# Optimization experiments

Measured on AMD Instinct MI355X. Metric: run time of the kernel, lower is better.

## Reference

```python
import jax, jax.numpy as jnp
import numpy as np

H = 8        # num_heads
D = 64       # qkv_dim
E = 512      # embed_dim = H*D
MS = 16      # ms_hidden_dim


def setup_inputs() -> dict:
    key = jax.random.key(0)
    ks = jax.random.split(key, 12)
    b, r, c = 4, 512, 512
    row_emb = jax.random.normal(ks[0], (b, r, E), dtype=jnp.float32)
    col_emb = jax.random.normal(ks[1], (b, c, E), dtype=jnp.float32)
    cost_mat = jax.random.uniform(ks[2], (b, r, c), dtype=jnp.float32)
    attn_mask = jax.random.randint(ks[3], (b, H, r, c), 0, 2) > 0
    s = 1.0 / np.sqrt(E)
    Wq = jax.random.uniform(ks[4], (H * D, E), minval=-s, maxval=s)
    Wk = jax.random.uniform(ks[5], (H * D, E), minval=-s, maxval=s)
    Wv = jax.random.uniform(ks[6], (H * D, E), minval=-s, maxval=s)
    Wout = jax.random.uniform(ks[7], (E, E), minval=-s, maxval=s)
    m1 = np.sqrt(0.5)
    m2 = np.sqrt(1.0 / MS)
    Wmix1 = jax.random.uniform(ks[8], (H * MS, 2 * H), minval=-m1, maxval=m1)
    Wmix2 = jax.random.uniform(ks[9], (H, H * MS), minval=-m2, maxval=m2)
    return {"row_emb": row_emb, "col_emb": col_emb, "cost_mat": cost_mat,
            "attn_mask": attn_mask, "Wq": Wq, "Wk": Wk, "Wv": Wv,
            "Wmix1": Wmix1, "Wmix2": Wmix2, "Wout": Wout}


def reference(row_emb, col_emb, cost_mat, attn_mask, Wq, Wk, Wv, Wmix1, Wmix2, Wout):
    b, r, _ = row_emb.shape
    c = col_emb.shape[1]
    norm = 1.0 / jnp.sqrt(jnp.asarray(D, row_emb.dtype))
    # projections -> [b, h, s, d]
    q = (row_emb @ Wq.T).reshape(b, r, H, D).transpose(0, 2, 1, 3)
    k = (col_emb @ Wk.T).reshape(b, c, H, D).transpose(0, 2, 1, 3)
    v = (col_emb @ Wv.T).reshape(b, c, H, D).transpose(0, 2, 1, 3)
    dot = norm * jnp.einsum('bhrd,bhcd->bhrc', q, k)            # [b,h,r,c]
    cost = jnp.broadcast_to(cost_mat[:, None, :, :], dot.shape)  # [b,h,r,c]
    # stack then rearrange 'b h r c s -> b r c (h s)' (h major, s minor)
    two = jnp.stack([dot, cost], axis=-1)                        # [b,h,r,c,2]
    two = two.transpose(0, 2, 3, 1, 4).reshape(b, r, c, 2 * H)
    hid = jax.nn.relu(two @ Wmix1.T)                             # [b,r,c,H*MS]
    ms = hid @ Wmix2.T                                           # [b,r,c,H]
    logits = ms.transpose(0, 3, 1, 2)                            # [b,h,r,c]
    # mask handling: rows that are fully masked become fully unmasked
    all_masked = jnp.all(attn_mask, axis=-1, keepdims=True)
    mask = jnp.where(all_masked, False, attn_mask)
    logits = jnp.where(mask, -jnp.inf, logits)
    weights = jax.nn.softmax(logits, axis=-1)
    out = jnp.einsum('bhrc,bhcd->bhrd', weights, v)              # [b,h,r,d]
    out = out.transpose(0, 2, 1, 3).reshape(b, r, H * D)         # b s (h d)
    return out @ Wout.T
```

## Files before the change

kernel.cpp:

```cpp
#include <hip/hip_runtime.h>
#include <math.h>

typedef __attribute__((ext_vector_type(8))) short bf16x8;
typedef __attribute__((ext_vector_type(4))) float f32x4;
typedef unsigned short ushort_t;

static __device__ inline unsigned short f2bf(float f) {
    union { float f; unsigned u; } v; v.f = f;
    unsigned r = v.u + 0x7fff + ((v.u >> 16) & 1);
    return (unsigned short)(r >> 16);
}

#if defined(__has_builtin)
#  if __has_builtin(__builtin_amdgcn_cvt_pk_bf16_f32)
#    define HAVE_PK_BF16 1
#  endif
#endif

static __device__ inline unsigned pk2bf(float a, float b) {
#ifdef HAVE_PK_BF16
    auto r = __builtin_amdgcn_cvt_pk_bf16_f32(a, b);
    unsigned u; __builtin_memcpy(&u, &r, 4);
    return u;
#else
    return (unsigned)f2bf(a) | ((unsigned)f2bf(b) << 16);
#endif
}

__global__ __launch_bounds__(256) void convert_allm(const float* __restrict__ a0,
                                                    const float* __restrict__ a1,
                                                    const float* __restrict__ a2,
                                                    const float* __restrict__ a3,
                                                    const float* __restrict__ a4,
                                                    const float* __restrict__ a5,
                                                    const int* __restrict__ mask,
                                                    ushort_t* __restrict__ dst,
                                                    int* __restrict__ allmOut) {
    if (blockIdx.x < 3072) {
        const size_t e = ((size_t)blockIdx.x * 256 + threadIdx.x) * 4;
        const float* src; size_t off;
        if      (e < 1048576) { src = a0; off = 0; }
        else if (e < 2097152) { src = a1; off = 1048576; }
        else if (e < 2359296) { src = a2; off = 2097152; }
        else if (e < 2621440) { src = a3; off = 2359296; }
        else if (e < 2883584) { src = a4; off = 2621440; }
        else                  { src = a5; off = 2883584; }
        const float4 v = *(const float4*)(src + (e - off));
        uint2 o; o.x = pk2bf(v.x, v.y); o.y = pk2bf(v.z, v.w);
        *(uint2*)(dst + e) = o;
    } else {
        const int bid  = blockIdx.x - 3072;
        const int w    = threadIdx.x >> 6;
        const int lane = threadIdx.x & 63;
        const int row  = bid * 4 + w;
        const int* mp = mask + (size_t)row * 512 + lane * 8;
        const int4 m0 = *(const int4*)mp;
        const int4 m1 = *(const int4*)(mp + 4);
        const int allv = (m0.x && m0.y && m0.z && m0.w &&
                          m1.x && m1.y && m1.z && m1.w);
        const int res = (__all(allv) != 0) ? 1 : 0;
        if (lane == 0) allmOut[row] = res;
    }
}

__global__ __launch_bounds__(256) void gemm_qkv(const ushort_t* __restrict__ rowb,
                                                const ushort_t* __restrict__ colb,
                                                const ushort_t* __restrict__ Wqb,
                                                const ushort_t* __restrict__ Wkb,
                                                const ushort_t* __restrict__ Wvb,
                                                ushort_t* __restrict__ Qb,
                                                ushort_t* __restrict__ Kb,
                                                ushort_t* __restrict__ Vt) {
    const int z = blockIdx.z;
    const ushort_t* A = (z == 0) ? rowb : colb;
    const ushort_t* B = (z == 0) ? Wqb : (z == 1) ? Wkb : Wvb;

    const int t    = threadIdx.x;
    const int w    = t >> 6;
    const int lane = t & 63;
    const int quad = lane >> 4;
    const int sl   = lane & 15;
    const int m0 = blockIdx.x * 64 + (w >> 1) * 32;
    const int n0 = blockIdx.y * 64 + (w & 1) * 32;

    const ushort_t* ap0 = A + (size_t)(m0 + sl) * 512 + quad * 8;
    const ushort_t* ap1 = A + (size_t)(m0 + 16 + sl) * 512 + quad * 8;
    const ushort_t* bp0 = B + (size_t)(n0 + sl) * 512 + quad * 8;
    const ushort_t* bp1 = B + (size_t)(n0 + 16 + sl) * 512 + quad * 8;

    f32x4 acc[2][2] = {};

    bf16x8 a0 = *(const bf16x8*)ap0;
    bf16x8 a1 = *(const bf16x8*)ap1;
    bf16x8 b0 = *(const bf16x8*)bp0;
    bf16x8 b1 = *(const bf16x8*)bp1;

    for (int ks = 0; ks < 16; ++ks) {
        bf16x8 na0, na1, nb0, nb1;
        if (ks < 15) {
            const int k0 = (ks + 1) * 32;
            na0 = *(const bf16x8*)(ap0 + k0);
            na1 = *(const bf16x8*)(ap1 + k0);
            nb0 = *(const bf16x8*)(bp0 + k0);
            nb1 = *(const bf16x8*)(bp1 + k0);
        }
        acc[0][0] = __builtin_amdgcn_mfma_f32_16x16x32_bf16(a0, b0, acc[0][0], 0, 0, 0);
        acc[0][1] = __builtin_amdgcn_mfma_f32_16x16x32_bf16(a0, b1, acc[0][1], 0, 0, 0);
        acc[1][0] = __builtin_amdgcn_mfma_f32_16x16x32_bf16(a1, b0, acc[1][0], 0, 0, 0);
        acc[1][1] = __builtin_amdgcn_mfma_f32_16x16x32_bf16(a1, b1, acc[1][1], 0, 0, 0);
        a0 = na0; a1 = na1; b0 = nb0; b1 = nb1;
    }

#pragma unroll
    for (int rs = 0; rs < 2; ++rs)
#pragma unroll
        for (int cs = 0; cs < 2; ++cs) {
            const int n = n0 + cs * 16 + sl;
            if (z == 2) {
                const int mb   = m0 + rs * 16 + quad * 4;
                const int bidx = mb >> 9, c = mb & 511;
                const int h = n >> 6, d = n & 63;
                ushort4 o;
                o.x = f2bf(acc[rs][cs][0]); o.y = f2bf(acc[rs][cs][1]);
                o.z = f2bf(acc[rs][cs][2]); o.w = f2bf(acc[rs][cs][3]);
                *(ushort4*)(Vt + (size_t)(((bidx * 8 + h) * 64 + d)) * 512 + c) = o;
            } else {
                ushort_t* C = (z == 0) ? Qb : Kb;
#pragma unroll
                for (int reg = 0; reg < 4; ++reg) {
                    const int m = m0 + rs * 16 + quad * 4 + reg;
                    C[(size_t)m * 512 + n] = f2bf(acc[rs][cs][reg]);
                }
            }
        }
}

__global__ __launch_bounds__(256) void gemm_out(const ushort_t* __restrict__ A,
                                                const ushort_t* __restrict__ B,
                                                float* __restrict__ C) {
    const int t    = threadIdx.x;
    const int w    = t >> 6;
    const int lane = t & 63;
    const int quad = lane >> 4;
    const int sl   = lane & 15;
    const int m0 = blockIdx.x * 64 + (w >> 1) * 32;
    const int n0 = blockIdx.y * 64 + (w & 1) * 32;

    const ushort_t* ap0 = A + (size_t)(m0 + sl) * 512 + quad * 8;
    const ushort_t* ap1 = A + (size_t)(m0 + 16 + sl) * 512 + quad * 8;
    const ushort_t* bp0 = B + (size_t)(n0 + sl) * 512 + quad * 8;
    const ushort_t* bp1 = B + (size_t)(n0 + 16 + sl) * 512 + quad * 8;

    f32x4 acc[2][2] = {};

    bf16x8 a0 = *(const bf16x8*)ap0;
    bf16x8 a1 = *(const bf16x8*)ap1;
    bf16x8 b0 = *(const bf16x8*)bp0;
    bf16x8 b1 = *(const bf16x8*)bp1;

    for (int ks = 0; ks < 16; ++ks) {
        bf16x8 na0, na1, nb0, nb1;
        if (ks < 15) {
            const int k0 = (ks + 1) * 32;
            na0 = *(const bf16x8*)(ap0 + k0);
            na1 = *(const bf16x8*)(ap1 + k0);
            nb0 = *(const bf16x8*)(bp0 + k0);
            nb1 = *(const bf16x8*)(bp1 + k0);
        }
        acc[0][0] = __builtin_amdgcn_mfma_f32_16x16x32_bf16(a0, b0, acc[0][0], 0, 0, 0);
        acc[0][1] = __builtin_amdgcn_mfma_f32_16x16x32_bf16(a0, b1, acc[0][1], 0, 0, 0);
        acc[1][0] = __builtin_amdgcn_mfma_f32_16x16x32_bf16(a1, b0, acc[1][0], 0, 0, 0);
        acc[1][1] = __builtin_amdgcn_mfma_f32_16x16x32_bf16(a1, b1, acc[1][1], 0, 0, 0);
        a0 = na0; a1 = na1; b0 = nb0; b1 = nb1;
    }

#pragma unroll
    for (int rs = 0; rs < 2; ++rs)
#pragma unroll
        for (int cs = 0; cs < 2; ++cs) {
            const int n = n0 + cs * 16 + sl;
#pragma unroll
            for (int reg = 0; reg < 4; ++reg) {
                const int m = m0 + rs * 16 + quad * 4 + reg;
                C[(size_t)m * 512 + n] = acc[rs][cs][reg];
            }
        }
}

__global__ __launch_bounds__(512) void dot_mlp_v7(const ushort_t* __restrict__ Qb,
                                                  const ushort_t* __restrict__ Kb,
                                                  const float* __restrict__ cost,
                                                  const float* __restrict__ W1,
                                                  const float* __restrict__ W2,
                                                  const int* __restrict__ mask,
                                                  const int* __restrict__ allm,
                                                  ushort_t* __restrict__ tbuf,
                                                  float* __restrict__ lpart) {
    __shared__ ushort_t Xs[1024 * 18];
    __shared__ ushort_t hidS[8 * 16 * 36];
    __shared__ ushort_t W1fs[128 * 16];
    __shared__ ushort_t W2ss[8 * 128];

    const int b  = blockIdx.z;
    const int r0 = blockIdx.y * 32;
    const int c0 = blockIdx.x * 32;
    const int t    = threadIdx.x;
    const int w    = t >> 6;
    const int lane = t & 63;
    const int quad = lane >> 4;
    const int sl   = lane & 15;

    const bf16x8 zf = {0, 0, 0, 0, 0, 0, 0, 0};

    if (t < 128) {
        float s = 0.f;
#pragma unroll
        for (int h = 0; h < 8; ++h) {
            W1fs[t * 16 + h] = f2bf(W1[t * 16 + 2 * h]);
            s += W1[t * 16 + 2 * h + 1];
        }
        W1fs[t * 16 + 8] = f2bf(s);
#pragma unroll
        for (int k = 9; k < 16; ++k) W1fs[t * 16 + k] = 0;
    }
#pragma unroll
    for (int i = 0; i < 2; ++i) W2ss[t + i * 512] = f2bf(W2[t + i * 512]);

#pragma unroll
    for (int i = 0; i < 2; ++i) {
        const int cell = t + i * 512;
        const int rl = cell >> 5, cl = cell & 31;
        unsigned* base = (unsigned*)(Xs + cell * 18 + 8);
        base[0] = (unsigned)f2bf(cost[((size_t)b * 512 + r0 + rl) * 512 + c0 + cl]);
        base[1] = 0; base[2] = 0; base[3] = 0; base[4] = 0;
    }

    {
        const int hp = w & 3;
        const int h0 = hp * 2;
        const int rs = w >> 2;
        bf16x8 af[2][2], bfr[2][2][2];
#pragma unroll
        for (int hh = 0; hh < 2; ++hh)
#pragma unroll
            for (int ks = 0; ks < 2; ++ks) {
                af[hh][ks] = *(const bf16x8*)(Qb +
                    ((size_t)(b * 512 + r0 + rs * 16 + sl) * 512 + (h0 + hh) * 64 + ks * 32 + quad * 8));
#pragma unroll
                for (int cs = 0; cs < 2; ++cs)
                    bfr[hh][cs][ks] = *(const bf16x8*)(Kb +
                        ((size_t)(b * 512 + c0 + cs * 16 + sl) * 512 + (h0 + hh) * 64 + ks * 32 + quad * 8));
            }
        f32x4 dacc[2][2];
#pragma unroll
        for (int hh = 0; hh < 2; ++hh)
#pragma unroll
            for (int cs = 0; cs < 2; ++cs) {
                f32x4 acc = {0.f, 0.f, 0.f, 0.f};
                acc = __builtin_amdgcn_mfma_f32_16x16x32_bf16(af[hh][0], bfr[hh][cs][0], acc, 0, 0, 0);
                acc = __builtin_amdgcn_mfma_f32_16x16x32_bf16(af[hh][1], bfr[hh][cs][1], acc, 0, 0, 0);
                dacc[hh][cs] = acc;
            }
#pragma unroll
        for (int cs = 0; cs < 2; ++cs)
#pragma unroll
            for (int reg = 0; reg < 4; ++reg) {
                const int cell = (rs * 16 + quad * 4 + reg) * 32 + cs * 16 + sl;
                ((unsigned*)Xs)[cell * 9 + hp] =
                    pk2bf(dacc[0][cs][reg] * 0.125f, dacc[1][cs][reg] * 0.125f);
            }
    }

    __syncthreads();

    bf16x8 bw1[8];
#pragma unroll
    for (int nt = 0; nt < 8; ++nt)
        bw1[nt] = (quad < 2) ? *(const bf16x8*)&W1fs[(nt * 16 + sl) * 16 + quad * 8] : zf;
    bf16x8 bw2[4];
#pragma unroll
    for (int ks = 0; ks < 4; ++ks) {
        union { ushort_t s[8]; bf16x8 v; } tu;
#pragma unroll
        for (int i = 0; i < 8; ++i) {
            const int p  = quad * 8 + i;
            const int jc = (p >> 1) | ((p & 1) << 4);
            tu.s[i] = (sl < 8) ? W2ss[sl * 128 + ks * 32 + jc] : (ushort_t)0;
        }
        bw2[ks] = tu.v;
    }

    ushort_t* hidW = hidS + w * (16 * 36);

    float rsum[4] = {0.f, 0.f, 0.f, 0.f};

#pragma unroll
    for (int mt = 0; mt < 8; ++mt) {
        const int gmt = w * 8 + mt;
        const int cb  = gmt * 16;

        bf16x8 a1 = zf;
        if (quad < 2) {
            const unsigned* xr = (const unsigned*)Xs + (size_t)(cb + sl) * 9 + quad * 4;
            union { unsigned u[4]; bf16x8 v; } tmp;
            tmp.u[0] = xr[0]; tmp.u[1] = xr[1]; tmp.u[2] = xr[2]; tmp.u[3] = xr[3];
            a1 = tmp.v;
        }

        f32x4 acc2 = {0.f, 0.f, 0.f, 0.f};
#pragma unroll
        for (int ks = 0; ks < 4; ++ks) {
            f32x4 z = {0.f, 0.f, 0.f, 0.f};
            const f32x4 h0 = __builtin_amdgcn_mfma_f32_16x16x32_bf16(a1, bw1[2 * ks],     z, 0, 0, 0);
            const f32x4 h1 = __builtin_amdgcn_mfma_f32_16x16x32_bf16(a1, bw1[2 * ks + 1], z, 0, 0, 0);
#pragma unroll
            for (int rp = 0; rp < 4; ++rp)
                ((unsigned*)hidW)[(quad * 4 + rp) * 18 + sl] =
                    pk2bf(fmaxf(h0[rp], 0.f), fmaxf(h1[rp], 0.f));
            union { uint2 u2[2]; bf16x8 v; } tu;
            const ushort_t* hp2 = hidW + sl * 36 + quad * 8;
            tu.u2[0] = *(const uint2*)hp2;
            tu.u2[1] = *(const uint2*)(hp2 + 4);
            acc2 = __builtin_amdgcn_mfma_f32_16x16x32_bf16(tu.v, bw2[ks], acc2, 0, 0, 0);
        }

        float psum = 0.f;
        if (sl < 8) {
            const int r = r0 + (gmt >> 1);
            const int cbase = c0 + (gmt & 1) * 16 + quad * 4;
            const size_t rowoff = (size_t)(b * 8 + sl) * 512 + r;
            const int4 m4 = *(const int4*)(mask + rowoff * 512 + cbase);
            const int av = allm[rowoff];
            float tv0 = (av || !m4.x) ? __expf(acc2[0]) : 0.f;
            float tv1 = (av || !m4.y) ? __expf(acc2[1]) : 0.f;
            float tv2 = (av || !m4.z) ? __expf(acc2[2]) : 0.f;
            float tv3 = (av || !m4.w) ? __expf(acc2[3]) : 0.f;
            ushort4 o;
            o.x = f2bf(tv0); o.y = f2bf(tv1); o.z = f2bf(tv2); o.w = f2bf(tv3);
            *(ushort4*)&tbuf[rowoff * 512 + cbase] = o;
            psum = tv0 + tv1 + tv2 + tv3;
        }
        psum += __shfl_xor(psum, 16, 64);
        psum += __shfl_xor(psum, 32, 64);
        rsum[mt >> 1] += psum;
    }

    if (quad == 0 && sl < 8) {
#pragma unroll
        for (int i = 0; i < 4; ++i) {
            const size_t rowoff = (size_t)(b * 8 + sl) * 512 + (r0 + w * 4 + i);
            lpart[rowoff * 16 + blockIdx.x] = rsum[i];
        }
    }
}

__global__ __launch_bounds__(256) void pv_norm(const ushort_t* __restrict__ tbuf,
                                               const float* __restrict__ lpart,
                                               const ushort_t* __restrict__ Vt,
                                               ushort_t* __restrict__ Aout) {
    __shared__ float lsum[16];

    const int t    = threadIdx.x;
    const int w    = t >> 6;
    const int lane = t & 63;
    const int quad = lane >> 4;
    const int sl   = lane & 15;
    const int rt = blockIdx.x;
    const int bh = blockIdx.y;
    const int r0 = rt * 16;

    if (t < 16) {
        const float* lp = lpart + ((size_t)bh * 512 + r0 + t) * 16;
        const float4 s0 = *(const float4*)lp;
        const float4 s1 = *(const float4*)(lp + 4);
        const float4 s2 = *(const float4*)(lp + 8);
        const float4 s3 = *(const float4*)(lp + 12);
        lsum[t] = (s0.x + s0.y + s0.z + s0.w) + (s1.x + s1.y + s1.z + s1.w) +
                  (s2.x + s2.y + s2.z + s2.w) + (s3.x + s3.y + s3.z + s3.w);
    }
    __syncthreads();

    const ushort_t* tb = tbuf + (size_t)bh * 512 * 512;
    const ushort_t* vb = Vt + (size_t)bh * 64 * 512;
    const int n0w = w * 16;

    f32x4 acc = {0.f, 0.f, 0.f, 0.f};
    for (int ks = 0; ks < 16; ++ks) {
        const bf16x8 ta = *(const bf16x8*)(tb + (size_t)(r0 + sl) * 512 + ks * 32 + quad * 8);
        const bf16x8 bv = *(const bf16x8*)(vb + (size_t)(n0w + sl) * 512 + ks * 32 + quad * 8);
        acc = __builtin_amdgcn_mfma_f32_16x16x32_bf16(ta, bv, acc, 0, 0, 0);
    }

    const int bidx = bh >> 3, h = bh & 7;
    ushort_t* Cb = Aout + (size_t)bidx * 512 * 512 + h * 64;
    const int n = n0w + sl;
#pragma unroll
    for (int reg = 0; reg < 4; ++reg) {
        const int m = r0 + quad * 4 + reg;
        const float inv = 1.f / lsum[quad * 4 + reg];
        Cb[(size_t)m * 512 + n] = f2bf(acc[reg] * inv);
    }
}

extern "C" void kernel_launch(void* const* d_in, const int* in_sizes, int n_in,
                              void* d_out, int out_size, void* d_ws, size_t ws_size,
                              hipStream_t stream) {
    const float* row_emb = (const float*)d_in[0];
    const float* col_emb = (const float*)d_in[1];
    const float* cost    = (const float*)d_in[2];
    const int*   mask    = (const int*)d_in[3];
    const float* Wq      = (const float*)d_in[4];
    const float* Wk      = (const float*)d_in[5];
    const float* Wv      = (const float*)d_in[6];
    const float* Wmix1   = (const float*)d_in[7];
    const float* Wmix2   = (const float*)d_in[8];
    const float* Wout    = (const float*)d_in[9];
    float* out = (float*)d_out;

    char* ws = (char*)d_ws;
    const size_t MB = (size_t)1 << 20;
    ushort_t* convDst = (ushort_t*)ws;
    ushort_t* rowb  = (ushort_t*)(ws);
    ushort_t* colb  = (ushort_t*)(ws + 2 * MB);
    ushort_t* Wqb   = (ushort_t*)(ws + 4 * MB);
    ushort_t* Wkb   = (ushort_t*)(ws + 4 * MB + 512 * 1024);
    ushort_t* Wvb   = (ushort_t*)(ws + 5 * MB);
    ushort_t* Woutb = (ushort_t*)(ws + 5 * MB + 512 * 1024);
    ushort_t* Qb    = (ushort_t*)(ws + 6 * MB);
    ushort_t* Kb    = (ushort_t*)(ws + 8 * MB);
    ushort_t* Vt    = (ushort_t*)(ws + 10 * MB);
    ushort_t* Aoutb = (ushort_t*)(ws + 12 * MB);
    ushort_t* tbuf  = (ushort_t*)(ws + 16 * MB);
    float* lpart    = (float*)(ws + 34 * MB);
    int* allmBuf    = (int*)(ws + 35 * MB);

    convert_allm<<<7168, 256, 0, stream>>>(row_emb, col_emb, Wq, Wk, Wv, Wout,
                                           mask, convDst, allmBuf);

    gemm_qkv<<<dim3(32, 8, 3), 256, 0, stream>>>(rowb, colb, Wqb, Wkb, Wvb, Qb, Kb, Vt);

    dot_mlp_v7<<<dim3(16, 16, 4), 512, 0, stream>>>(Qb, Kb, cost, Wmix1, Wmix2,
                                                    mask, allmBuf, tbuf, lpart);

    pv_norm<<<dim3(32, 32), 256, 0, stream>>>(tbuf, lpart, Vt, Aoutb);

    gemm_out<<<dim3(32, 8), 256, 0, stream>>>(Aoutb, Woutb, out);
}
```

Baseline: 193.2 us.

## Pack attention mask into bitmask, split-K accumulators in GEMMs, smaller gemm_out tiles

The mask pre-pass now packs each row's int32 mask into a bitmask with the fully-masked-row rule folded in, so the MLP/softmax kernel reads one 32-bit word instead of an int4 plus a separate flag. That cuts mask traffic in the hot kernel roughly 32-fold. Both GEMMs split K into two independent accumulator chains to expose more MFMA parallelism and in-flight loads. gemm_out also drops to 32x32 tiles, launching four times as many blocks for better occupancy, at the cost of less operand reuse.

```diff
diff --git a/kernel.cpp b/kernel.cpp
--- a/kernel.cpp
+++ b/kernel.cpp
@@ -35,7 +35,7 @@
                                                     const float* __restrict__ a5,
                                                     const int* __restrict__ mask,
                                                     ushort_t* __restrict__ dst,
-                                                    int* __restrict__ allmOut) {
+                                                    unsigned char* __restrict__ bmask) {
     if (blockIdx.x < 3072) {
         const size_t e = ((size_t)blockIdx.x * 256 + threadIdx.x) * 4;
         const float* src; size_t off;
@@ -56,10 +56,17 @@
         const int* mp = mask + (size_t)row * 512 + lane * 8;
         const int4 m0 = *(const int4*)mp;
         const int4 m1 = *(const int4*)(mp + 4);
-        const int allv = (m0.x && m0.y && m0.z && m0.w &&
-                          m1.x && m1.y && m1.z && m1.w);
-        const int res = (__all(allv) != 0) ? 1 : 0;
-        if (lane == 0) allmOut[row] = res;
+        unsigned bits = 0;
+        bits |= (m0.x != 0) ? 1u   : 0u;
+        bits |= (m0.y != 0) ? 2u   : 0u;
+        bits |= (m0.z != 0) ? 4u   : 0u;
+        bits |= (m0.w != 0) ? 8u   : 0u;
+        bits |= (m1.x != 0) ? 16u  : 0u;
+        bits |= (m1.y != 0) ? 32u  : 0u;
+        bits |= (m1.z != 0) ? 64u  : 0u;
+        bits |= (m1.w != 0) ? 128u : 0u;
+        const bool all_masked = (__all(bits == 255u) != 0);
+        bmask[(size_t)row * 64 + lane] = all_masked ? 0 : (unsigned char)bits;
     }
 }
 
@@ -88,48 +95,54 @@
     const ushort_t* bp0 = B + (size_t)(n0 + sl) * 512 + quad * 8;
     const ushort_t* bp1 = B + (size_t)(n0 + 16 + sl) * 512 + quad * 8;
 
-    f32x4 acc[2][2] = {};
-
-    bf16x8 a0 = *(const bf16x8*)ap0;
-    bf16x8 a1 = *(const bf16x8*)ap1;
-    bf16x8 b0 = *(const bf16x8*)bp0;
-    bf16x8 b1 = *(const bf16x8*)bp1;
-
-    for (int ks = 0; ks < 16; ++ks) {
-        bf16x8 na0, na1, nb0, nb1;
-        if (ks < 15) {
-            const int k0 = (ks + 1) * 32;
-            na0 = *(const bf16x8*)(ap0 + k0);
-            na1 = *(const bf16x8*)(ap1 + k0);
-            nb0 = *(const bf16x8*)(bp0 + k0);
-            nb1 = *(const bf16x8*)(bp1 + k0);
-        }
-        acc[0][0] = __builtin_amdgcn_mfma_f32_16x16x32_bf16(a0, b0, acc[0][0], 0, 0, 0);
-        acc[0][1] = __builtin_amdgcn_mfma_f32_16x16x32_bf16(a0, b1, acc[0][1], 0, 0, 0);
-        acc[1][0] = __builtin_amdgcn_mfma_f32_16x16x32_bf16(a1, b0, acc[1][0], 0, 0, 0);
-        acc[1][1] = __builtin_amdgcn_mfma_f32_16x16x32_bf16(a1, b1, acc[1][1], 0, 0, 0);
-        a0 = na0; a1 = na1; b0 = nb0; b1 = nb1;
+    f32x4 accA[2][2] = {}, accB[2][2] = {};
+
+    bf16x8 a0A = *(const bf16x8*)ap0,         a1A = *(const bf16x8*)ap1;
+    bf16x8 b0A = *(const bf16x8*)bp0,         b1A = *(const bf16x8*)bp1;
+    bf16x8 a0B = *(const bf16x8*)(ap0 + 256), a1B = *(const bf16x8*)(ap1 + 256);
+    bf16x8 b0B = *(const bf16x8*)(bp0 + 256), b1B = *(const bf16x8*)(bp1 + 256);
+
+    for (int ks = 0; ks < 8; ++ks) {
+        bf16x8 na0A, na1A, nb0A, nb1A, na0B, na1B, nb0B, nb1B;
+        if (ks < 7) {
+            const int o = (ks + 1) * 32;
+            na0A = *(const bf16x8*)(ap0 + o);       na1A = *(const bf16x8*)(ap1 + o);
+            nb0A = *(const bf16x8*)(bp0 + o);       nb1A = *(const bf16x8*)(bp1 + o);
+            na0B = *(const bf16x8*)(ap0 + 256 + o); na1B = *(const bf16x8*)(ap1 + 256 + o);
+            nb0B = *(const bf16x8*)(bp0 + 256 + o); nb1B = *(const bf16x8*)(bp1 + 256 + o);
+        }
+        accA[0][0] = __builtin_amdgcn_mfma_f32_16x16x32_bf16(a0A, b0A, accA[0][0], 0, 0, 0);
+        accA[0][1] = __builtin_amdgcn_mfma_f32_16x16x32_bf16(a0A, b1A, accA[0][1], 0, 0, 0);
+        accA[1][0] = __builtin_amdgcn_mfma_f32_16x16x32_bf16(a1A, b0A, accA[1][0], 0, 0, 0);
+        accA[1][1] = __builtin_amdgcn_mfma_f32_16x16x32_bf16(a1A, b1A, accA[1][1], 0, 0, 0);
+        accB[0][0] = __builtin_amdgcn_mfma_f32_16x16x32_bf16(a0B, b0B, accB[0][0], 0, 0, 0);
+        accB[0][1] = __builtin_amdgcn_mfma_f32_16x16x32_bf16(a0B, b1B, accB[0][1], 0, 0, 0);
+        accB[1][0] = __builtin_amdgcn_mfma_f32_16x16x32_bf16(a1B, b0B, accB[1][0], 0, 0, 0);
+        accB[1][1] = __builtin_amdgcn_mfma_f32_16x16x32_bf16(a1B, b1B, accB[1][1], 0, 0, 0);
+        a0A = na0A; a1A = na1A; b0A = nb0A; b1A = nb1A;
+        a0B = na0B; a1B = na1B; b0B = nb0B; b1B = nb1B;
     }
 
 #pragma unroll
     for (int rs = 0; rs < 2; ++rs)
 #pragma unroll
         for (int cs = 0; cs < 2; ++cs) {
+            const f32x4 acc = accA[rs][cs] + accB[rs][cs];
             const int n = n0 + cs * 16 + sl;
             if (z == 2) {
                 const int mb   = m0 + rs * 16 + quad * 4;
                 const int bidx = mb >> 9, c = mb & 511;
                 const int h = n >> 6, d = n & 63;
                 ushort4 o;
-                o.x = f2bf(acc[rs][cs][0]); o.y = f2bf(acc[rs][cs][1]);
-                o.z = f2bf(acc[rs][cs][2]); o.w = f2bf(acc[rs][cs][3]);
+                o.x = f2bf(acc[0]); o.y = f2bf(acc[1]);
+                o.z = f2bf(acc[2]); o.w = f2bf(acc[3]);
                 *(ushort4*)(Vt + (size_t)(((bidx * 8 + h) * 64 + d)) * 512 + c) = o;
             } else {
                 ushort_t* C = (z == 0) ? Qb : Kb;
 #pragma unroll
                 for (int reg = 0; reg < 4; ++reg) {
                     const int m = m0 + rs * 16 + quad * 4 + reg;
-                    C[(size_t)m * 512 + n] = f2bf(acc[rs][cs][reg]);
+                    C[(size_t)m * 512 + n] = f2bf(acc[reg]);
                 }
             }
         }
@@ -143,57 +156,44 @@
     const int lane = t & 63;
     const int quad = lane >> 4;
     const int sl   = lane & 15;
-    const int m0 = blockIdx.x * 64 + (w >> 1) * 32;
-    const int n0 = blockIdx.y * 64 + (w & 1) * 32;
-
-    const ushort_t* ap0 = A + (size_t)(m0 + sl) * 512 + quad * 8;
-    const ushort_t* ap1 = A + (size_t)(m0 + 16 + sl) * 512 + quad * 8;
-    const ushort_t* bp0 = B + (size_t)(n0 + sl) * 512 + quad * 8;
-    const ushort_t* bp1 = B + (size_t)(n0 + 16 + sl) * 512 + quad * 8;
-
-    f32x4 acc[2][2] = {};
-
-    bf16x8 a0 = *(const bf16x8*)ap0;
-    bf16x8 a1 = *(const bf16x8*)ap1;
-    bf16x8 b0 = *(const bf16x8*)bp0;
-    bf16x8 b1 = *(const bf16x8*)bp1;
-
-    for (int ks = 0; ks < 16; ++ks) {
-        bf16x8 na0, na1, nb0, nb1;
-        if (ks < 15) {
-            const int k0 = (ks + 1) * 32;
-            na0 = *(const bf16x8*)(ap0 + k0);
-            na1 = *(const bf16x8*)(ap1 + k0);
-            nb0 = *(const bf16x8*)(bp0 + k0);
-            nb1 = *(const bf16x8*)(bp1 + k0);
-        }
-        acc[0][0] = __builtin_amdgcn_mfma_f32_16x16x32_bf16(a0, b0, acc[0][0], 0, 0, 0);
-        acc[0][1] = __builtin_amdgcn_mfma_f32_16x16x32_bf16(a0, b1, acc[0][1], 0, 0, 0);
-        acc[1][0] = __builtin_amdgcn_mfma_f32_16x16x32_bf16(a1, b0, acc[1][0], 0, 0, 0);
-        acc[1][1] = __builtin_amdgcn_mfma_f32_16x16x32_bf16(a1, b1, acc[1][1], 0, 0, 0);
-        a0 = na0; a1 = na1; b0 = nb0; b1 = nb1;
-    }
-
-#pragma unroll
-    for (int rs = 0; rs < 2; ++rs)
-#pragma unroll
-        for (int cs = 0; cs < 2; ++cs) {
-            const int n = n0 + cs * 16 + sl;
-#pragma unroll
-            for (int reg = 0; reg < 4; ++reg) {
-                const int m = m0 + rs * 16 + quad * 4 + reg;
-                C[(size_t)m * 512 + n] = acc[rs][cs][reg];
-            }
-        }
-}
-
-__global__ __launch_bounds__(512) void dot_mlp_v7(const ushort_t* __restrict__ Qb,
+    const int m0 = blockIdx.x * 32 + (w >> 1) * 16;
+    const int n0 = blockIdx.y * 32 + (w & 1) * 16;
+
+    const ushort_t* ap = A + (size_t)(m0 + sl) * 512 + quad * 8;
+    const ushort_t* bp = B + (size_t)(n0 + sl) * 512 + quad * 8;
+
+    f32x4 accA = {0.f, 0.f, 0.f, 0.f}, accB = {0.f, 0.f, 0.f, 0.f};
+
+    bf16x8 aA = *(const bf16x8*)ap,         bA = *(const bf16x8*)bp;
+    bf16x8 aB = *(const bf16x8*)(ap + 256), bB = *(const bf16x8*)(bp + 256);
+
+    for (int ks = 0; ks < 8; ++ks) {
+        bf16x8 naA, nbA, naB, nbB;
+        if (ks < 7) {
+            const int o = (ks + 1) * 32;
+            naA = *(const bf16x8*)(ap + o);       nbA = *(const bf16x8*)(bp + o);
+            naB = *(const bf16x8*)(ap + 256 + o); nbB = *(const bf16x8*)(bp + 256 + o);
+        }
+        accA = __builtin_amdgcn_mfma_f32_16x16x32_bf16(aA, bA, accA, 0, 0, 0);
+        accB = __builtin_amdgcn_mfma_f32_16x16x32_bf16(aB, bB, accB, 0, 0, 0);
+        aA = naA; bA = nbA; aB = naB; bB = nbB;
+    }
+
+    const f32x4 acc = accA + accB;
+    const int n = n0 + sl;
+#pragma unroll
+    for (int reg = 0; reg < 4; ++reg) {
+        const int m = m0 + quad * 4 + reg;
+        C[(size_t)m * 512 + n] = acc[reg];
+    }
+}
+
+__global__ __launch_bounds__(512) void dot_mlp_v8(const ushort_t* __restrict__ Qb,
                                                   const ushort_t* __restrict__ Kb,
                                                   const float* __restrict__ cost,
                                                   const float* __restrict__ W1,
                                                   const float* __restrict__ W2,
-                                                  const int* __restrict__ mask,
-                                                  const int* __restrict__ allm,
+                                                  const unsigned* __restrict__ bmask,
                                                   ushort_t* __restrict__ tbuf,
                                                   float* __restrict__ lpart) {
     __shared__ ushort_t Xs[1024 * 18];
@@ -329,12 +329,12 @@
             const int r = r0 + (gmt >> 1);
             const int cbase = c0 + (gmt & 1) * 16 + quad * 4;
             const size_t rowoff = (size_t)(b * 8 + sl) * 512 + r;
-            const int4 m4 = *(const int4*)(mask + rowoff * 512 + cbase);
-            const int av = allm[rowoff];
-            float tv0 = (av || !m4.x) ? __expf(acc2[0]) : 0.f;
-            float tv1 = (av || !m4.y) ? __expf(acc2[1]) : 0.f;
-            float tv2 = (av || !m4.z) ? __expf(acc2[2]) : 0.f;
-            float tv3 = (av || !m4.w) ? __expf(acc2[3]) : 0.f;
+            const unsigned mw = bmask[rowoff * 16 + (c0 >> 5)];
+            const unsigned bits = (mw >> ((gmt & 1) * 16 + quad * 4)) & 0xFu;
+            float tv0 = (bits & 1u) ? 0.f : __expf(acc2[0]);
+            float tv1 = (bits & 2u) ? 0.f : __expf(acc2[1]);
+            float tv2 = (bits & 4u) ? 0.f : __expf(acc2[2]);
+            float tv3 = (bits & 8u) ? 0.f : __expf(acc2[3]);
             ushort4 o;
             o.x = f2bf(tv0); o.y = f2bf(tv1); o.z = f2bf(tv2); o.w = f2bf(tv3);
             *(ushort4*)&tbuf[rowoff * 512 + cbase] = o;
@@ -432,17 +432,17 @@
     ushort_t* Aoutb = (ushort_t*)(ws + 12 * MB);
     ushort_t* tbuf  = (ushort_t*)(ws + 16 * MB);
     float* lpart    = (float*)(ws + 34 * MB);
-    int* allmBuf    = (int*)(ws + 35 * MB);
+    unsigned char* bmaskBuf = (unsigned char*)(ws + 35 * MB);
 
     convert_allm<<<7168, 256, 0, stream>>>(row_emb, col_emb, Wq, Wk, Wv, Wout,
-                                           mask, convDst, allmBuf);
+                                           mask, convDst, bmaskBuf);
 
     gemm_qkv<<<dim3(32, 8, 3), 256, 0, stream>>>(rowb, colb, Wqb, Wkb, Wvb, Qb, Kb, Vt);
 
-    dot_mlp_v7<<<dim3(16, 16, 4), 512, 0, stream>>>(Qb, Kb, cost, Wmix1, Wmix2,
-                                                    mask, allmBuf, tbuf, lpart);
+    dot_mlp_v8<<<dim3(16, 16, 4), 512, 0, stream>>>(Qb, Kb, cost, Wmix1, Wmix2,
+                                                    (const unsigned*)bmaskBuf, tbuf, lpart);
 
     pv_norm<<<dim3(32, 32), 256, 0, stream>>>(tbuf, lpart, Vt, Aoutb);
 
-    gemm_out<<<dim3(32, 8), 256, 0, stream>>>(Aoutb, Woutb, out);
-}
+    gemm_out<<<dim3(64, 16), 256, 0, stream>>>(Aoutb, Woutb, out);
+}
```

Measured after the change: 200.5 us. 1.04x slower.
